# Optimization experiments

Measured on AMD Instinct MI355X. Metric: run time of the kernel, lower is better.

The kernel has to match this reference:

```python
import jax, jax.numpy as jnp
import numpy as np

B_SZ, C_IN, C_OUT, H, W = 16, 32, 32, 128, 128
K, CODE, PAD, FACTOR = 3, 2, 1, 1.0

def setup_inputs() -> dict:
    key = jax.random.key(0)
    ks = jax.random.split(key, 7)
    s = 0.05
    return {
        "x": jax.random.normal(ks[0], (B_SZ, C_IN, H, W), jnp.float32),
        "codes": jax.random.normal(ks[1], (B_SZ, CODE, CODE), jnp.float32),
        "weight": jax.random.normal(ks[2], (C_OUT, C_IN, K, K), jnp.float32) * s,
        "A": jax.random.normal(ks[3], (C_IN, CODE, K, K), jnp.float32) * s,
        "Bm": jax.random.normal(ks[4], (C_OUT, CODE, K, K), jnp.float32) * s,
        "bias": jax.random.normal(ks[5], (C_OUT,), jnp.float32) * s,
        "bias_context": jax.random.normal(ks[6], (CODE, C_OUT), jnp.float32) * s,
    }

def reference(x, codes, weight, A, Bm, bias, bias_context):
    # hypernetwork weight synthesis: [b, out, in, k, k]
    w_ctx = jnp.einsum('ickl,bcr->birkl', A, codes)            # [b, in, code, k, k]
    w_ctx = jnp.einsum('birkl,orkl->boikl', w_ctx, Bm)         # [b, out, in, k, k]
    combined_weight = weight[None] + FACTOR * w_ctx
    # per-sample bias from diagonal of codes
    diag = jnp.diagonal(codes, axis1=-2, axis2=-1)             # [b, code]
    combined_bias = bias[None] + FACTOR * (diag @ bias_context)  # [b, out]
    # circular padding then per-sample VALID conv (== unfold + einsum)
    xp = jnp.pad(x, ((0, 0), (0, 0), (PAD, PAD), (PAD, PAD)), mode='wrap')
    def conv_one(xi, wi):
        return jax.lax.conv_general_dilated(
            xi[None], wi, window_strides=(1, 1), padding='VALID',
            dimension_numbers=('NCHW', 'OIHW', 'NCHW'))[0]
    out = jax.vmap(conv_one)(xp, combined_weight)              # [b, out, H, W]
    return out + combined_bias[:, :, None, None]
```

## Files before the change

kernel.cpp:

```cpp
#include <hip/hip_runtime.h>

typedef short bf16x8 __attribute__((ext_vector_type(8)));
typedef float f32x4  __attribute__((ext_vector_type(4)));
typedef unsigned short u16;
typedef unsigned int   u32;

#define HH 128
#define WW 128

__device__ __forceinline__ u16 f2bf(float f) {
    union { float f; u32 i; } v; v.f = f;
    u32 x = v.i;
    x += 0x7fffu + ((x >> 16) & 1u);
    return (u16)(x >> 16);
}

__global__ __launch_bounds__(512, 2) void geps_mfma_kernel(
    const float* __restrict__ x, const float* __restrict__ codes,
    const float* __restrict__ weight, const float* __restrict__ A,
    const float* __restrict__ Bm, const float* __restrict__ bias,
    const float* __restrict__ bctx, float* __restrict__ out)
{
    __shared__ bf16x8 lds_x[3072];
    __shared__ bf16x8 lds_w[1152];
    __shared__ float  lds_ctx[576];
    __shared__ float  lds_b[32];

    const int tid  = threadIdx.x;
    const int l    = tid & 63;
    const int wvid = tid >> 6;
    const int row  = wvid >> 1;
    const int oh   = wvid & 1;

    const int orig = blockIdx.x;
    const int vb   = (orig & 7) * 64 + (orig >> 3);
    const int rb   = vb & 31;
    const int b    = vb >> 5;
    const int h0   = rb * 4;

    const float c00 = codes[b * 4 + 0];
    const float c01 = codes[b * 4 + 1];
    const float c10 = codes[b * 4 + 2];
    const float c11 = codes[b * 4 + 3];

    for (int j = tid; j < 576; j += 512) {
        int i = j / 18, rem = j % 18, r = rem / 9, kl = rem % 9;
        float a0 = A[(i * 2 + 0) * 9 + kl];
        float a1 = A[(i * 2 + 1) * 9 + kl];
        lds_ctx[j] = (r == 0) ? (a0 * c00 + a1 * c10) : (a0 * c01 + a1 * c11);
    }
    if (tid < 32) lds_b[tid] = bias[tid] + c00 * bctx[tid] + c11 * bctx[32 + tid];
    __syncthreads();

    for (int j = tid; j < 1152; j += 512) {
        int kl = j >> 7, rem = j & 127, o = rem >> 2, kb = rem & 3;
        float m0 = Bm[(o * 2 + 0) * 9 + kl];
        float m1 = Bm[(o * 2 + 1) * 9 + kl];
        bf16x8 w8;
        #pragma unroll
        for (int jj = 0; jj < 8; ++jj) {
            int i = kb * 8 + jj;
            float wf = weight[(o * 32 + i) * 9 + kl]
                     + lds_ctx[(i * 2 + 0) * 9 + kl] * m0
                     + lds_ctx[(i * 2 + 1) * 9 + kl] * m1;
            w8[jj] = (short)f2bf(wf);
        }
        lds_w[kl * 128 + (o >> 4) * 64 + kb * 16 + (o & 15)] = w8;
    }

    #pragma unroll
    for (int it = 0; it < 3; ++it) {
        int idx = it * 512 + tid;
        int cp  = idx & 63;
        int ig  = (idx >> 6) & 3;
        int rr  = idx >> 8;
        int c0  = cp * 2;
        int grow = (h0 - 1 + rr) & 127;
        const float* src = x + ((size_t)(b * 32 + ig * 8) * HH + grow) * WW + c0;
        bf16x8 v0, v1;
        #pragma unroll
        for (int jj = 0; jj < 8; ++jj) {
            float2 f = *(const float2*)(src + (size_t)jj * HH * WW);
            v0[jj] = (short)f2bf(f.x);
            v1[jj] = (short)f2bf(f.y);
        }
        int didx = rr * 512 + (c0 >> 4) * 64 + ig * 16 + (c0 & 15);
        lds_x[didx]     = v0;
        lds_x[didx + 1] = v1;
    }
    __syncthreads();

    const int awb = oh * 64 + (l >> 4) * 16 + (l & 15);
    bf16x8 af[9];
    #pragma unroll
    for (int kl = 0; kl < 9; ++kl)
        af[kl] = lds_w[kl * 128 + awb];

    const int p = l & 15, igf = l >> 4;
    int bb[3];
    #pragma unroll
    for (int dl = -1; dl <= 1; ++dl) {
        int pq = p + dl;
        bb[dl + 1] = (pq & 15) + ((pq >> 4) << 6) + igf * 16;
    }

    f32x4 acc[8];
    #pragma unroll
    for (int nt = 0; nt < 8; ++nt) acc[nt] = (f32x4){0.f, 0.f, 0.f, 0.f};

    #pragma unroll
    for (int nt = 0; nt < 8; ++nt) {
        #pragma unroll
        for (int lc = 0; lc < 3; ++lc) {
            int t = (bb[lc] + nt * 64) & 511;
            #pragma unroll
            for (int k = 0; k < 3; ++k) {
                bf16x8 bfv = lds_x[(row + k) * 512 + t];
                acc[nt] = __builtin_amdgcn_mfma_f32_16x16x32_bf16(
                    af[k * 3 + lc], bfv, acc[nt], 0, 0, 0);
            }
        }
    }

    float blr[4];
    #pragma unroll
    for (int r = 0; r < 4; ++r) blr[r] = lds_b[oh * 16 + (l >> 4) * 4 + r];

    const int h = h0 + row;
    const size_t obase = ((size_t)(b * 32 + oh * 16 + (l >> 4) * 4) * HH + h) * WW + p;
    #pragma unroll
    for (int nt = 0; nt < 8; ++nt)
        #pragma unroll
        for (int r = 0; r < 4; ++r)
            out[obase + (size_t)r * (HH * WW) + nt * 16] = acc[nt][r] + blr[r];
}

extern "C" void kernel_launch(void* const* d_in, const int* in_sizes, int n_in,
                              void* d_out, int out_size, void* d_ws, size_t ws_size,
                              hipStream_t stream) {
    const float* x      = (const float*)d_in[0];
    const float* codes  = (const float*)d_in[1];
    const float* weight = (const float*)d_in[2];
    const float* A      = (const float*)d_in[3];
    const float* Bm     = (const float*)d_in[4];
    const float* bias   = (const float*)d_in[5];
    const float* bctx   = (const float*)d_in[6];
    float* out = (float*)d_out;

    hipLaunchKernelGGL(geps_mfma_kernel, dim3(512), dim3(512), 0, stream,
                       x, codes, weight, A, Bm, bias, bctx, out);
}
```

Baseline: 26.17 us.

## Process two row tiles per block with register prefetch and packed bf16 conversion

Each block now handles two 4-row tiles of the same sample (h0 and h0+64) and launches 256 blocks instead of 512, so the synthesized per-sample weights are computed once per two tiles. The second tile's input is prefetched into registers while the first tile's MFMA work runs, then converted and written to LDS. Software f32-to-bf16 rounding is replaced with the hardware v_cvt_pk_bf16_f32 instruction, and LDS stores are widened to 128-bit. The trade-off is half as many blocks, launch bounds lowered to one block per CU, and higher register pressure from the 24-float2 prefetch buffer, which could reduce latency hiding.

```diff
diff --git a/kernel.cpp b/kernel.cpp
--- a/kernel.cpp
+++ b/kernel.cpp
@@ -8,14 +8,13 @@
 #define HH 128
 #define WW 128
 
-__device__ __forceinline__ u16 f2bf(float f) {
-    union { float f; u32 i; } v; v.f = f;
-    u32 x = v.i;
-    x += 0x7fffu + ((x >> 16) & 1u);
-    return (u16)(x >> 16);
+__device__ __forceinline__ u32 cvt_pk_bf16(float lo, float hi) {
+    u32 r;
+    asm volatile("v_cvt_pk_bf16_f32 %0, %1, %2" : "=v"(r) : "v"(lo), "v"(hi));
+    return r;
 }
 
-__global__ __launch_bounds__(512, 2) void geps_mfma_kernel(
+__global__ __launch_bounds__(512, 1) void geps_mfma_kernel(
     const float* __restrict__ x, const float* __restrict__ codes,
     const float* __restrict__ weight, const float* __restrict__ A,
     const float* __restrict__ Bm, const float* __restrict__ bias,
@@ -33,10 +32,11 @@
     const int oh   = wvid & 1;
 
     const int orig = blockIdx.x;
-    const int vb   = (orig & 7) * 64 + (orig >> 3);
-    const int rb   = vb & 31;
-    const int b    = vb >> 5;
-    const int h0   = rb * 4;
+    const int vb   = (orig & 7) * 32 + (orig >> 3);
+    const int b    = vb >> 4;
+    const int pair = vb & 15;
+    const int h0   = pair * 4;
+    const int h1   = h0 + 64;
 
     const float c00 = codes[b * 4 + 0];
     const float c01 = codes[b * 4 + 1];
@@ -56,16 +56,19 @@
         int kl = j >> 7, rem = j & 127, o = rem >> 2, kb = rem & 3;
         float m0 = Bm[(o * 2 + 0) * 9 + kl];
         float m1 = Bm[(o * 2 + 1) * 9 + kl];
-        bf16x8 w8;
+        float wf[8];
         #pragma unroll
         for (int jj = 0; jj < 8; ++jj) {
             int i = kb * 8 + jj;
-            float wf = weight[(o * 32 + i) * 9 + kl]
-                     + lds_ctx[(i * 2 + 0) * 9 + kl] * m0
-                     + lds_ctx[(i * 2 + 1) * 9 + kl] * m1;
-            w8[jj] = (short)f2bf(wf);
+            wf[jj] = weight[(o * 32 + i) * 9 + kl]
+                   + lds_ctx[i * 18 + kl] * m0
+                   + lds_ctx[i * 18 + 9 + kl] * m1;
         }
-        lds_w[kl * 128 + (o >> 4) * 64 + kb * 16 + (o & 15)] = w8;
+        u32 pk[4];
+        #pragma unroll
+        for (int q = 0; q < 4; ++q) pk[q] = cvt_pk_bf16(wf[2 * q], wf[2 * q + 1]);
+        *(uint4*)&lds_w[kl * 128 + (o >> 4) * 64 + kb * 16 + (o & 15)] =
+            make_uint4(pk[0], pk[1], pk[2], pk[3]);
     }
 
     #pragma unroll
@@ -77,16 +80,19 @@
         int c0  = cp * 2;
         int grow = (h0 - 1 + rr) & 127;
         const float* src = x + ((size_t)(b * 32 + ig * 8) * HH + grow) * WW + c0;
-        bf16x8 v0, v1;
+        float2 f[8];
         #pragma unroll
-        for (int jj = 0; jj < 8; ++jj) {
-            float2 f = *(const float2*)(src + (size_t)jj * HH * WW);
-            v0[jj] = (short)f2bf(f.x);
-            v1[jj] = (short)f2bf(f.y);
+        for (int jj = 0; jj < 8; ++jj)
+            f[jj] = *(const float2*)(src + (size_t)jj * HH * WW);
+        u32 p0[4], p1[4];
+        #pragma unroll
+        for (int q = 0; q < 4; ++q) {
+            p0[q] = cvt_pk_bf16(f[2 * q].x, f[2 * q + 1].x);
+            p1[q] = cvt_pk_bf16(f[2 * q].y, f[2 * q + 1].y);
         }
         int didx = rr * 512 + (c0 >> 4) * 64 + ig * 16 + (c0 & 15);
-        lds_x[didx]     = v0;
-        lds_x[didx + 1] = v1;
+        *(uint4*)&lds_x[didx]     = make_uint4(p0[0], p0[1], p0[2], p0[3]);
+        *(uint4*)&lds_x[didx + 1] = make_uint4(p1[0], p1[1], p1[2], p1[3]);
     }
     __syncthreads();
 
@@ -104,35 +110,75 @@
         bb[dl + 1] = (pq & 15) + ((pq >> 4) << 6) + igf * 16;
     }
 
-    f32x4 acc[8];
-    #pragma unroll
-    for (int nt = 0; nt < 8; ++nt) acc[nt] = (f32x4){0.f, 0.f, 0.f, 0.f};
-
-    #pragma unroll
-    for (int nt = 0; nt < 8; ++nt) {
-        #pragma unroll
-        for (int lc = 0; lc < 3; ++lc) {
-            int t = (bb[lc] + nt * 64) & 511;
-            #pragma unroll
-            for (int k = 0; k < 3; ++k) {
-                bf16x8 bfv = lds_x[(row + k) * 512 + t];
-                acc[nt] = __builtin_amdgcn_mfma_f32_16x16x32_bf16(
-                    af[k * 3 + lc], bfv, acc[nt], 0, 0, 0);
-            }
-        }
-    }
-
     float blr[4];
     #pragma unroll
     for (int r = 0; r < 4; ++r) blr[r] = lds_b[oh * 16 + (l >> 4) * 4 + r];
 
-    const int h = h0 + row;
-    const size_t obase = ((size_t)(b * 32 + oh * 16 + (l >> 4) * 4) * HH + h) * WW + p;
+    auto compute_store = [&](int hbase) {
+        f32x4 acc[8];
+        #pragma unroll
+        for (int nt = 0; nt < 8; ++nt) acc[nt] = (f32x4){0.f, 0.f, 0.f, 0.f};
+        #pragma unroll
+        for (int nt = 0; nt < 8; ++nt) {
+            #pragma unroll
+            for (int lc = 0; lc < 3; ++lc) {
+                int t = (bb[lc] + nt * 64) & 511;
+                #pragma unroll
+                for (int k = 0; k < 3; ++k) {
+                    bf16x8 bfv = lds_x[(row + k) * 512 + t];
+                    acc[nt] = __builtin_amdgcn_mfma_f32_16x16x32_bf16(
+                        af[k * 3 + lc], bfv, acc[nt], 0, 0, 0);
+                }
+            }
+        }
+        const int h = hbase + row;
+        const size_t obase =
+            ((size_t)(b * 32 + oh * 16 + (l >> 4) * 4) * HH + h) * WW + p;
+        #pragma unroll
+        for (int nt = 0; nt < 8; ++nt)
+            #pragma unroll
+            for (int r = 0; r < 4; ++r)
+                out[obase + (size_t)r * (HH * WW) + nt * 16] = acc[nt][r] + blr[r];
+    };
+
+    float2 pf[24];
     #pragma unroll
-    for (int nt = 0; nt < 8; ++nt)
+    for (int it = 0; it < 3; ++it) {
+        int idx = it * 512 + tid;
+        int cp  = idx & 63;
+        int ig  = (idx >> 6) & 3;
+        int rr  = idx >> 8;
+        int grow = (h1 - 1 + rr) & 127;
+        const float* src = x + ((size_t)(b * 32 + ig * 8) * HH + grow) * WW + cp * 2;
         #pragma unroll
-        for (int r = 0; r < 4; ++r)
-            out[obase + (size_t)r * (HH * WW) + nt * 16] = acc[nt][r] + blr[r];
+        for (int jj = 0; jj < 8; ++jj)
+            pf[it * 8 + jj] = *(const float2*)(src + (size_t)jj * HH * WW);
+    }
+
+    compute_store(h0);
+
+    __syncthreads();
+
+    #pragma unroll
+    for (int it = 0; it < 3; ++it) {
+        int idx = it * 512 + tid;
+        int cp  = idx & 63;
+        int ig  = (idx >> 6) & 3;
+        int rr  = idx >> 8;
+        int c0  = cp * 2;
+        u32 p0[4], p1[4];
+        #pragma unroll
+        for (int q = 0; q < 4; ++q) {
+            p0[q] = cvt_pk_bf16(pf[it * 8 + 2 * q].x, pf[it * 8 + 2 * q + 1].x);
+            p1[q] = cvt_pk_bf16(pf[it * 8 + 2 * q].y, pf[it * 8 + 2 * q + 1].y);
+        }
+        int didx = rr * 512 + (c0 >> 4) * 64 + ig * 16 + (c0 & 15);
+        *(uint4*)&lds_x[didx]     = make_uint4(p0[0], p0[1], p0[2], p0[3]);
+        *(uint4*)&lds_x[didx + 1] = make_uint4(p1[0], p1[1], p1[2], p1[3]);
+    }
+    __syncthreads();
+
+    compute_store(h1);
 }
 
 extern "C" void kernel_launch(void* const* d_in, const int* in_sizes, int n_in,
@@ -147,6 +193,6 @@
     const float* bctx   = (const float*)d_in[6];
     float* out = (float*)d_out;
 
-    hipLaunchKernelGGL(geps_mfma_kernel, dim3(512), dim3(512), 0, stream,
+    hipLaunchKernelGGL(geps_mfma_kernel, dim3(256), dim3(512), 0, stream,
                        x, codes, weight, A, Bm, bias, bctx, out);
 }
```

Result: faster. 24.49 us (-6.4%).
